# Optimization experiments

Hardware: AMD Instinct MI355X
Metric: run time of the kernel (lower is better)

## Reference

```python
import jax, jax.numpy as jnp
import numpy as np

N_NODES = 50000
N_EDGES = 800000
D = 128


def _gcn_conv(x, edge_index, W, b):
    """PyG GCNConv: out = D^{-1/2} (A + I) D^{-1/2} (x W) + b.

    edge_index[0] = source nodes, edge_index[1] = target nodes.
    Self-loops handled analytically instead of materializing them.
    """
    n = x.shape[0]
    src, dst = edge_index[0], edge_index[1]
    h = x @ W  # [N, out]
    # degree with self-loop: in-degree of target + 1
    deg = jax.ops.segment_sum(jnp.ones_like(dst, dtype=h.dtype), dst, num_segments=n) + 1.0
    dinv = jax.lax.rsqrt(deg)  # deg >= 1, safe
    norm = dinv[src] * dinv[dst]  # [E]
    msgs = norm[:, None] * h[src]  # [E, out]  (the big irregular-gather intermediate)
    agg = jax.ops.segment_sum(msgs, dst, num_segments=n)
    # self-loop contribution: norm = dinv[i]*dinv[i] = 1/deg
    agg = agg + h * (1.0 / deg)[:, None]
    return agg + b


def setup_inputs() -> dict:
    key = jax.random.key(0)
    k1, k2, k3, k4 = jax.random.split(key, 4)
    x = jax.random.normal(k1, (N_NODES, D), dtype=jnp.float32)
    edge_index = jax.random.randint(k2, (2, N_EDGES), 0, N_NODES, dtype=jnp.int64)
    scale = 1.0 / np.sqrt(D)
    W1 = jax.random.normal(k3, (D, D), dtype=jnp.float32) * scale
    W2 = jax.random.normal(k4, (D, D), dtype=jnp.float32) * scale
    b1 = jnp.zeros((D,), dtype=jnp.float32)
    b2 = jnp.zeros((D,), dtype=jnp.float32)
    return {"x": x, "edge_index": edge_index, "W1": W1, "b1": b1, "W2": W2, "b2": b2}


def reference(x, edge_index, W1, b1, W2, b2):
    h = _gcn_conv(x, edge_index, W1, b1)
    h = jax.nn.relu(h)  # dropout p=0.0 -> identity
    out = _gcn_conv(h, edge_index, W2, b2)
    return out
```

## Files before the change

### kernel.cpp

```cpp
#include <hip/hip_runtime.h>

#define DF 128
#define NBKT_MAX 256
#define CAP 8192

typedef unsigned int uint;
typedef unsigned short ushort;
typedef __attribute__((ext_vector_type(8))) short short8;
typedef __attribute__((ext_vector_type(4))) float f32x4;

union frag_u { uint4 u4; short8 s8; };

__device__ __forceinline__ uint f2u(float f) { return __float_as_uint(f); }
__device__ __forceinline__ ushort rne_bf16(float v) {
    uint u = __float_as_uint(v);
    u = u + 0x7FFFu + ((u >> 16) & 1u);
    return (ushort)(u >> 16);
}
__device__ __forceinline__ float bflo(uint u) { return __uint_as_float(u << 16); }
__device__ __forceinline__ float bfhi(uint u) { return __uint_as_float(u & 0xFFFF0000u); }

__global__ __launch_bounds__(256) void scatter_wprep(const int* __restrict__ src,
                                                     const int* __restrict__ dst,
                                                     int* __restrict__ ccur,
                                                     uint* __restrict__ ebuf,
                                                     int E, int NB, int SB,
                                                     const float* __restrict__ W1,
                                                     const float* __restrict__ W2,
                                                     uint4* __restrict__ Whi,
                                                     uint4* __restrict__ Wlo) {
    __shared__ int cnt[NBKT_MAX];
    __shared__ int base[NBKT_MAX];
    int t = threadIdx.x;
    if ((int)blockIdx.x < SB) {
        int e0 = blockIdx.x * 8192, e1 = min(E, e0 + 8192);
        for (int i = t; i < NB; i += 256) cnt[i] = 0;
        __syncthreads();
        for (int e = e0 + t; e < e1; e += 256) atomicAdd(&cnt[dst[e] >> 8], 1);
        __syncthreads();
        for (int i = t; i < NB; i += 256) base[i] = cnt[i] ? atomicAdd(&ccur[i], cnt[i]) : 0;
        __syncthreads();
        for (int e = e0 + t; e < e1; e += 256) {
            int d = dst[e];
            int b = d >> 8;
            int pos = atomicAdd(&base[b], 1);
            if (pos < CAP) ebuf[(size_t)b * CAP + pos] = ((uint)(d & 255) << 24) | (uint)src[e];
        }
    } else {
        int tt4 = ((int)blockIdx.x - SB) * 256 + t;
        int wsel = tt4 >> 11;
        int tt = tt4 & 2047;
        const float* W = wsel ? W2 : W1;
        int lane = tt & 63;
        int n  = ((tt >> 6) & 7) * 16 + (lane & 15);
        int k0 = (tt >> 9) * 32 + (lane >> 4) * 8;
        uint hi[4], lo[4];
#pragma unroll
        for (int p = 0; p < 4; ++p) {
            float f0 = W[(size_t)(k0 + 2 * p) * DF + n];
            float f1 = W[(size_t)(k0 + 2 * p + 1) * DF + n];
            uint u0 = f2u(f0), u1 = f2u(f1);
            hi[p] = (u1 & 0xFFFF0000u) | (u0 >> 16);
            float l0 = f0 - __uint_as_float(u0 & 0xFFFF0000u);
            float l1 = f1 - __uint_as_float(u1 & 0xFFFF0000u);
            lo[p] = (f2u(l1) & 0xFFFF0000u) | (f2u(l0) >> 16);
        }
        Whi[wsel * 2048 + tt] = make_uint4(hi[0], hi[1], hi[2], hi[3]);
        Wlo[wsel * 2048 + tt] = make_uint4(lo[0], lo[1], lo[2], lo[3]);
    }
}

__global__ __launch_bounds__(256) void sort_gemm1(const uint* __restrict__ ebuf,
                                                  const int* __restrict__ ccur,
                                                  int* __restrict__ rstart,
                                                  int* __restrict__ rend,
                                                  float* __restrict__ dinv,
                                                  ushort* __restrict__ srcs,
                                                  int* __restrict__ perm,
                                                  const float* __restrict__ A,
                                                  const uint4* __restrict__ Bhi,
                                                  const uint4* __restrict__ Blo,
                                                  ushort* __restrict__ Hq,
                                                  int NB, int N) {
    __shared__ int cnt[256];
    __shared__ int sp[256];
    __shared__ ushort prm[256];
    int t = threadIdx.x;
    if ((int)blockIdx.x < NB) {
        int b = blockIdx.x;
        int count = min(ccur[b], CAP);
        const uint* eb = ebuf + (size_t)b * CAP;
        cnt[t] = 0;
        __syncthreads();
        for (int j = t; j < count; j += 256) atomicAdd(&cnt[eb[j] >> 24], 1);
        __syncthreads();
        int v = cnt[t];
        sp[t] = v;
        __syncthreads();
        for (int off = 1; off < 256; off <<= 1) {
            int x = (t >= off) ? sp[t - off] : 0;
            __syncthreads();
            sp[t] += x;
            __syncthreads();
        }
        int ex = sp[t] - v;
        int node = b * 256 + t;
        if (node < N) {
            rstart[node] = b * CAP + ex;
            rend[node]   = b * CAP + ex + v;
            dinv[node] = rsqrtf((float)v + 1.0f);
        }
        int rank = 0;
#pragma unroll 8
        for (int u = 0; u < 256; ++u) {
            int du = cnt[u];
            rank += (du > v) || (du == v && u < t);
        }
        prm[rank] = (ushort)t;
        sp[t] = ex;
        __syncthreads();
        perm[b * 256 + t] = b * 256 + (int)prm[t];
        for (int j = t; j < count; j += 256) {
            uint e = eb[j];
            int pos = atomicAdd(&sp[e >> 24], 1);
            srcs[(size_t)b * CAP + pos] = (ushort)(e & 0xFFFFFFu);
        }
    } else {
        const int lane = t & 63;
        const int w = t >> 6;
        const int l15 = lane & 15, quad = lane >> 4;
        const int rowbase = ((int)blockIdx.x - NB) * 128 + w * 32;
        const int M = N;

        f32x4 acc[2][8];
#pragma unroll
        for (int rt = 0; rt < 2; ++rt)
#pragma unroll
            for (int ct = 0; ct < 8; ++ct) acc[rt][ct] = (f32x4){0.f, 0.f, 0.f, 0.f};

        for (int q = 0; q < 4; ++q) {
            frag_u ah[2], al[2];
#pragma unroll
            for (int rt = 0; rt < 2; ++rt) {
                int m = rowbase + rt * 16 + l15;
                if (m >= M) m = M - 1;
                const float* ap = A + (size_t)m * DF + q * 32 + quad * 8;
                float4 v0 = *(const float4*)ap;
                float4 v1 = *(const float4*)(ap + 4);
                float f[8] = {v0.x, v0.y, v0.z, v0.w, v1.x, v1.y, v1.z, v1.w};
                uint hi[4], lo[4];
#pragma unroll
                for (int p = 0; p < 4; ++p) {
                    uint u0 = f2u(f[2 * p]), u1 = f2u(f[2 * p + 1]);
                    hi[p] = (u1 & 0xFFFF0000u) | (u0 >> 16);
                    float l0 = f[2 * p]     - __uint_as_float(u0 & 0xFFFF0000u);
                    float l1 = f[2 * p + 1] - __uint_as_float(u1 & 0xFFFF0000u);
                    lo[p] = (f2u(l1) & 0xFFFF0000u) | (f2u(l0) >> 16);
                }
                ah[rt].u4 = make_uint4(hi[0], hi[1], hi[2], hi[3]);
                al[rt].u4 = make_uint4(lo[0], lo[1], lo[2], lo[3]);
            }
#pragma unroll
            for (int ct = 0; ct < 8; ++ct) {
                frag_u bh, bl;
                bh.u4 = Bhi[(q * 8 + ct) * 64 + lane];
                bl.u4 = Blo[(q * 8 + ct) * 64 + lane];
#pragma unroll
                for (int rt = 0; rt < 2; ++rt) {
                    acc[rt][ct] = __builtin_amdgcn_mfma_f32_16x16x32_bf16(al[rt].s8, bh.s8, acc[rt][ct], 0, 0, 0);
                    acc[rt][ct] = __builtin_amdgcn_mfma_f32_16x16x32_bf16(ah[rt].s8, bl.s8, acc[rt][ct], 0, 0, 0);
                    acc[rt][ct] = __builtin_amdgcn_mfma_f32_16x16x32_bf16(ah[rt].s8, bh.s8, acc[rt][ct], 0, 0, 0);
                }
            }
        }
#pragma unroll
        for (int rt = 0; rt < 2; ++rt)
#pragma unroll
            for (int reg = 0; reg < 4; ++reg) {
                int row = rowbase + rt * 16 + quad * 4 + reg;
                if (row < M) {
#pragma unroll
                    for (int ct = 0; ct < 8; ++ct)
                        Hq[((size_t)(ct >> 1) * M + row) * 32 + (ct & 1) * 16 + l15] =
                            rne_bf16(acc[rt][ct][reg]);
                }
            }
    }
}

__global__ __launch_bounds__(256) void gemm_bf16A(const ushort* __restrict__ A,
                                                  const uint4* __restrict__ Bhi,
                                                  const uint4* __restrict__ Blo,
                                                  const float* __restrict__ dinv,
                                                  ushort* __restrict__ Hq, int M) {
    const int lane = threadIdx.x & 63;
    const int w = threadIdx.x >> 6;
    const int l15 = lane & 15, quad = lane >> 4;
    const int rowbase = blockIdx.x * 128 + w * 32;

    f32x4 acc[2][8];
#pragma unroll
    for (int rt = 0; rt < 2; ++rt)
#pragma unroll
        for (int ct = 0; ct < 8; ++ct) acc[rt][ct] = (f32x4){0.f, 0.f, 0.f, 0.f};

    for (int q = 0; q < 4; ++q) {
        frag_u a[2];
#pragma unroll
        for (int rt = 0; rt < 2; ++rt) {
            int m = rowbase + rt * 16 + l15;
            if (m >= M) m = M - 1;
            const ushort* ap = A + ((size_t)q * M + m) * 32 + quad * 8;
            a[rt].u4 = *(const uint4*)ap;
        }
#pragma unroll
        for (int ct = 0; ct < 8; ++ct) {
            frag_u bh, bl;
            bh.u4 = Bhi[(q * 8 + ct) * 64 + lane];
            bl.u4 = Blo[(q * 8 + ct) * 64 + lane];
#pragma unroll
            for (int rt = 0; rt < 2; ++rt) {
                acc[rt][ct] = __builtin_amdgcn_mfma_f32_16x16x32_bf16(a[rt].s8, bl.s8, acc[rt][ct], 0, 0, 0);
                acc[rt][ct] = __builtin_amdgcn_mfma_f32_16x16x32_bf16(a[rt].s8, bh.s8, acc[rt][ct], 0, 0, 0);
            }
        }
    }
#pragma unroll
    for (int rt = 0; rt < 2; ++rt)
#pragma unroll
        for (int reg = 0; reg < 4; ++reg) {
            int row = rowbase + rt * 16 + quad * 4 + reg;
            if (row < M) {
                float di = dinv[row];
#pragma unroll
                for (int ct = 0; ct < 8; ++ct)
                    Hq[((size_t)(ct >> 1) * M + row) * 32 + (ct & 1) * 16 + l15] =
                        rne_bf16(acc[rt][ct][reg] * di);
            }
        }
}

template<bool L1>
__global__ __launch_bounds__(256) void quarter_gather(const uint4* __restrict__ H4,
                                                      const float* __restrict__ dinv,
                                                      const int* __restrict__ rstart,
                                                      const int* __restrict__ rend,
                                                      const ushort* __restrict__ srcs,
                                                      const int* __restrict__ perm,
                                                      const float* __restrict__ bias,
                                                      void* __restrict__ outv, int N) {
    int t = threadIdx.x;
    int bid = blockIdx.x;
    int sub = bid & 7;
    int q = sub >> 1;
    int slot = (bid >> 3) * 128 + (sub & 1) * 64 + (t >> 2);
    int n = perm[slot];
    if (n >= N) return;
    int l = t & 3;
    const uint4* Hq4 = H4 + (size_t)q * N * 4;

    float4 bb0 = ((const float4*)bias)[q * 8 + l * 2];
    float4 bb1 = ((const float4*)bias)[q * 8 + l * 2 + 1];

    float di = dinv[n];
    uint4 self = Hq4[(size_t)n * 4 + l];
    float sc = L1 ? di : 1.0f;
    float a0 = bflo(self.x) * sc, a1 = bfhi(self.x) * sc, a2 = bflo(self.y) * sc, a3 = bfhi(self.y) * sc;
    float a4 = bflo(self.z) * sc, a5 = bfhi(self.z) * sc, a6 = bflo(self.w) * sc, a7 = bfhi(self.w) * sc;

    int j = rstart[n], end = rend[n];
    for (; j + 4 <= end; j += 4) {
        int s0 = srcs[j], s1 = srcs[j + 1], s2 = srcs[j + 2], s3 = srcs[j + 3];
        uint4 v0 = Hq4[(size_t)s0 * 4 + l];
        uint4 v1 = Hq4[(size_t)s1 * 4 + l];
        uint4 v2 = Hq4[(size_t)s2 * 4 + l];
        uint4 v3 = Hq4[(size_t)s3 * 4 + l];
        if constexpr (L1) {
            float d0 = dinv[s0], d1 = dinv[s1], d2 = dinv[s2], d3 = dinv[s3];
            a0 = fmaf(bflo(v0.x), d0, a0); a0 = fmaf(bflo(v1.x), d1, a0);
            a0 = fmaf(bflo(v2.x), d2, a0); a0 = fmaf(bflo(v3.x), d3, a0);
            a1 = fmaf(bfhi(v0.x), d0, a1); a1 = fmaf(bfhi(v1.x), d1, a1);
            a1 = fmaf(bfhi(v2.x), d2, a1); a1 = fmaf(bfhi(v3.x), d3, a1);
            a2 = fmaf(bflo(v0.y), d0, a2); a2 = fmaf(bflo(v1.y), d1, a2);
            a2 = fmaf(bflo(v2.y), d2, a2); a2 = fmaf(bflo(v3.y), d3, a2);
            a3 = fmaf(bfhi(v0.y), d0, a3); a3 = fmaf(bfhi(v1.y), d1, a3);
            a3 = fmaf(bfhi(v2.y), d2, a3); a3 = fmaf(bfhi(v3.y), d3, a3);
            a4 = fmaf(bflo(v0.z), d0, a4); a4 = fmaf(bflo(v1.z), d1, a4);
            a4 = fmaf(bflo(v2.z), d2, a4); a4 = fmaf(bflo(v3.z), d3, a4);
            a5 = fmaf(bfhi(v0.z), d0, a5); a5 = fmaf(bfhi(v1.z), d1, a5);
            a5 = fmaf(bfhi(v2.z), d2, a5); a5 = fmaf(bfhi(v3.z), d3, a5);
            a6 = fmaf(bflo(v0.w), d0, a6); a6 = fmaf(bflo(v1.w), d1, a6);
            a6 = fmaf(bflo(v2.w), d2, a6); a6 = fmaf(bflo(v3.w), d3, a6);
            a7 = fmaf(bfhi(v0.w), d0, a7); a7 = fmaf(bfhi(v1.w), d1, a7);
            a7 = fmaf(bfhi(v2.w), d2, a7); a7 = fmaf(bfhi(v3.w), d3, a7);
        } else {
            a0 += (bflo(v0.x) + bflo(v1.x)) + (bflo(v2.x) + bflo(v3.x));
            a1 += (bfhi(v0.x) + bfhi(v1.x)) + (bfhi(v2.x) + bfhi(v3.x));
            a2 += (bflo(v0.y) + bflo(v1.y)) + (bflo(v2.y) + bflo(v3.y));
            a3 += (bfhi(v0.y) + bfhi(v1.y)) + (bfhi(v2.y) + bfhi(v3.y));
            a4 += (bflo(v0.z) + bflo(v1.z)) + (bflo(v2.z) + bflo(v3.z));
            a5 += (bfhi(v0.z) + bfhi(v1.z)) + (bfhi(v2.z) + bfhi(v3.z));
            a6 += (bflo(v0.w) + bflo(v1.w)) + (bflo(v2.w) + bflo(v3.w));
            a7 += (bfhi(v0.w) + bfhi(v1.w)) + (bfhi(v2.w) + bfhi(v3.w));
        }
    }
    for (; j < end; ++j) {
        int s = srcs[j];
        uint4 v = Hq4[(size_t)s * 4 + l];
        if constexpr (L1) {
            float d = dinv[s];
            a0 = fmaf(bflo(v.x), d, a0); a1 = fmaf(bfhi(v.x), d, a1);
            a2 = fmaf(bflo(v.y), d, a2); a3 = fmaf(bfhi(v.y), d, a3);
            a4 = fmaf(bflo(v.z), d, a4); a5 = fmaf(bfhi(v.z), d, a5);
            a6 = fmaf(bflo(v.w), d, a6); a7 = fmaf(bfhi(v.w), d, a7);
        } else {
            a0 += bflo(v.x); a1 += bfhi(v.x); a2 += bflo(v.y); a3 += bfhi(v.y);
            a4 += bflo(v.z); a5 += bfhi(v.z); a6 += bflo(v.w); a7 += bfhi(v.w);
        }
    }
    float o0 = fmaf(a0, di, bb0.x), o1 = fmaf(a1, di, bb0.y);
    float o2 = fmaf(a2, di, bb0.z), o3 = fmaf(a3, di, bb0.w);
    float o4 = fmaf(a4, di, bb1.x), o5 = fmaf(a5, di, bb1.y);
    float o6 = fmaf(a6, di, bb1.z), o7 = fmaf(a7, di, bb1.w);
    if (L1) {
        o0 = fmaxf(o0, 0.f); o1 = fmaxf(o1, 0.f); o2 = fmaxf(o2, 0.f); o3 = fmaxf(o3, 0.f);
        o4 = fmaxf(o4, 0.f); o5 = fmaxf(o5, 0.f); o6 = fmaxf(o6, 0.f); o7 = fmaxf(o7, 0.f);
        uint4 pk;
        pk.x = (uint)rne_bf16(o0) | ((uint)rne_bf16(o1) << 16);
        pk.y = (uint)rne_bf16(o2) | ((uint)rne_bf16(o3) << 16);
        pk.z = (uint)rne_bf16(o4) | ((uint)rne_bf16(o5) << 16);
        pk.w = (uint)rne_bf16(o6) | ((uint)rne_bf16(o7) << 16);
        ((uint4*)outv)[((size_t)q * N + n) * 4 + l] = pk;
    } else {
        float4* op = (float4*)((float*)outv + (size_t)n * DF + q * 32 + l * 8);
        op[0] = make_float4(o0, o1, o2, o3);
        op[1] = make_float4(o4, o5, o6, o7);
    }
}

extern "C" void kernel_launch(void* const* d_in, const int* in_sizes, int n_in,
                              void* d_out, int out_size, void* d_ws, size_t ws_size,
                              hipStream_t stream) {
    const float* x  = (const float*)d_in[0];
    const int*   ei = (const int*)d_in[1];
    const float* W1 = (const float*)d_in[2];
    const float* b1 = (const float*)d_in[3];
    const float* W2 = (const float*)d_in[4];
    const float* b2 = (const float*)d_in[5];

    const int N = in_sizes[0] / DF;
    const int E = in_sizes[1] / 2;
    const int* src = ei;
    const int* dstp = ei + E;
    const int NB = (N + 255) >> 8;
    const int SB = (E + 8191) / 8192;

    float* out = (float*)d_out;
    char* ws = (char*)d_ws;
    size_t off = 0;
    auto carve = [&](size_t bytes) { void* p = ws + off; off += (bytes + 255) & ~(size_t)255; return p; };
    ushort* Hq     = (ushort*)carve((size_t)N * DF * sizeof(ushort));
    ushort* Z1     = (ushort*)carve((size_t)N * DF * sizeof(ushort));
    float*  dinv   = (float*)carve((size_t)N * sizeof(float));
    int*    rstart = (int*)carve((size_t)N * sizeof(int));
    int*    rend   = (int*)carve((size_t)N * sizeof(int));
    int*    perm   = (int*)carve((size_t)NB * 256 * sizeof(int));
    uint*   ebuf   = (uint*)carve((size_t)NB * CAP * sizeof(uint));
    ushort* srcs   = (ushort*)carve((size_t)NB * CAP * sizeof(ushort));
    int*    ccur   = (int*)carve(NBKT_MAX * sizeof(int));
    uint4*  Whi    = (uint4*)carve(2 * 2048 * sizeof(uint4));
    uint4*  Wlo    = (uint4*)carve(2 * 2048 * sizeof(uint4));

    const int gemm_b = (N + 127) / 128;
    const int gath_b = ((N + 127) / 128) * 8;

    hipMemsetAsync(ccur, 0, NBKT_MAX * sizeof(int), stream);
    scatter_wprep<<<SB + 16, 256, 0, stream>>>(src, dstp, ccur, ebuf, E, NB, SB, W1, W2, Whi, Wlo);

    sort_gemm1<<<NB + gemm_b, 256, 0, stream>>>(ebuf, ccur, rstart, rend, dinv, srcs, perm,
                                                x, Whi, Wlo, Hq, NB, N);

    quarter_gather<true><<<gath_b, 256, 0, stream>>>((const uint4*)Hq, dinv, rstart, rend,
                                                     srcs, perm, b1, Z1, N);

    gemm_bf16A<<<gemm_b, 256, 0, stream>>>(Z1, Whi + 2048, Wlo + 2048, dinv, Hq, N);
    quarter_gather<false><<<gath_b, 256, 0, stream>>>((const uint4*)Hq, dinv, rstart, rend,
                                                      srcs, perm, b2, out, N);
}
```

Baseline: 234.9 us.

## Pad CSR rows to 8, vectorize edge loads, drop degree-sorted permutation

The scatter kernel now processes smaller edge chunks with each thread loading 8 edges through int4 vector loads. In the sort stage each node's edge segment is padded to a multiple of 8, which aligns row starts so the gather can read 8 source indices with one uint4 load and issue 8 row fetches at once. The degree-sorted permutation used for load balancing is removed, so gather blocks map nodes directly. This trades warp-level balance across nodes of differing degree for more memory-level parallelism and fewer index loads. Padding also uses more bucket capacity, and any edges beyond CAP are now dropped silently.

```diff
diff --git a/kernel.cpp b/kernel.cpp
--- a/kernel.cpp
+++ b/kernel.cpp
@@ -3,6 +3,7 @@
 #define DF 128
 #define NBKT_MAX 256
 #define CAP 8192
+#define SCHUNK 2048
 
 typedef unsigned int uint;
 typedef unsigned short ushort;
@@ -33,19 +34,34 @@
     __shared__ int base[NBKT_MAX];
     int t = threadIdx.x;
     if ((int)blockIdx.x < SB) {
-        int e0 = blockIdx.x * 8192, e1 = min(E, e0 + 8192);
+        int e0 = blockIdx.x * SCHUNK;
+        int eb0 = e0 + t * 8;
+        int lim = min(E - eb0, 8);
+        int d[8], s[8];
+        if (lim == 8) {
+            int4 d0 = *(const int4*)(dst + eb0), d1 = *(const int4*)(dst + eb0 + 4);
+            int4 s0 = *(const int4*)(src + eb0), s1 = *(const int4*)(src + eb0 + 4);
+            d[0] = d0.x; d[1] = d0.y; d[2] = d0.z; d[3] = d0.w;
+            d[4] = d1.x; d[5] = d1.y; d[6] = d1.z; d[7] = d1.w;
+            s[0] = s0.x; s[1] = s0.y; s[2] = s0.z; s[3] = s0.w;
+            s[4] = s1.x; s[5] = s1.y; s[6] = s1.z; s[7] = s1.w;
+        } else {
+            for (int i = 0; i < 8; ++i) { d[i] = 0; s[i] = 0; }
+            for (int i = 0; i < lim; ++i) { d[i] = dst[eb0 + i]; s[i] = src[eb0 + i]; }
+        }
         for (int i = t; i < NB; i += 256) cnt[i] = 0;
         __syncthreads();
-        for (int e = e0 + t; e < e1; e += 256) atomicAdd(&cnt[dst[e] >> 8], 1);
+        for (int i = 0; i < 8; ++i)
+            if (i < lim) atomicAdd(&cnt[d[i] >> 8], 1);
         __syncthreads();
         for (int i = t; i < NB; i += 256) base[i] = cnt[i] ? atomicAdd(&ccur[i], cnt[i]) : 0;
         __syncthreads();
-        for (int e = e0 + t; e < e1; e += 256) {
-            int d = dst[e];
-            int b = d >> 8;
-            int pos = atomicAdd(&base[b], 1);
-            if (pos < CAP) ebuf[(size_t)b * CAP + pos] = ((uint)(d & 255) << 24) | (uint)src[e];
-        }
+        for (int i = 0; i < 8; ++i)
+            if (i < lim) {
+                int b = d[i] >> 8;
+                int pos = atomicAdd(&base[b], 1);
+                if (pos < CAP) ebuf[(size_t)b * CAP + pos] = ((uint)(d[i] & 255) << 24) | (uint)s[i];
+            }
     } else {
         int tt4 = ((int)blockIdx.x - SB) * 256 + t;
         int wsel = tt4 >> 11;
@@ -76,7 +92,6 @@
                                                   int* __restrict__ rend,
                                                   float* __restrict__ dinv,
                                                   ushort* __restrict__ srcs,
-                                                  int* __restrict__ perm,
                                                   const float* __restrict__ A,
                                                   const uint4* __restrict__ Bhi,
                                                   const uint4* __restrict__ Blo,
@@ -84,7 +99,6 @@
                                                   int NB, int N) {
     __shared__ int cnt[256];
     __shared__ int sp[256];
-    __shared__ ushort prm[256];
     int t = threadIdx.x;
     if ((int)blockIdx.x < NB) {
         int b = blockIdx.x;
@@ -95,7 +109,8 @@
         for (int j = t; j < count; j += 256) atomicAdd(&cnt[eb[j] >> 24], 1);
         __syncthreads();
         int v = cnt[t];
-        sp[t] = v;
+        int pv = (v + 7) & ~7;
+        sp[t] = pv;
         __syncthreads();
         for (int off = 1; off < 256; off <<= 1) {
             int x = (t >= off) ? sp[t - off] : 0;
@@ -103,27 +118,19 @@
             sp[t] += x;
             __syncthreads();
         }
-        int ex = sp[t] - v;
+        int ex = sp[t] - pv;
         int node = b * 256 + t;
         if (node < N) {
             rstart[node] = b * CAP + ex;
             rend[node]   = b * CAP + ex + v;
             dinv[node] = rsqrtf((float)v + 1.0f);
         }
-        int rank = 0;
-#pragma unroll 8
-        for (int u = 0; u < 256; ++u) {
-            int du = cnt[u];
-            rank += (du > v) || (du == v && u < t);
-        }
-        prm[rank] = (ushort)t;
         sp[t] = ex;
         __syncthreads();
-        perm[b * 256 + t] = b * 256 + (int)prm[t];
         for (int j = t; j < count; j += 256) {
             uint e = eb[j];
             int pos = atomicAdd(&sp[e >> 24], 1);
-            srcs[(size_t)b * CAP + pos] = (ushort)(e & 0xFFFFFFu);
+            if (pos < CAP) srcs[(size_t)b * CAP + pos] = (ushort)(e & 0xFFFFFFu);
         }
     } else {
         const int lane = t & 63;
@@ -246,15 +253,13 @@
                                                       const int* __restrict__ rstart,
                                                       const int* __restrict__ rend,
                                                       const ushort* __restrict__ srcs,
-                                                      const int* __restrict__ perm,
                                                       const float* __restrict__ bias,
                                                       void* __restrict__ outv, int N) {
     int t = threadIdx.x;
     int bid = blockIdx.x;
     int sub = bid & 7;
     int q = sub >> 1;
-    int slot = (bid >> 3) * 128 + (sub & 1) * 64 + (t >> 2);
-    int n = perm[slot];
+    int n = (bid >> 3) * 128 + (sub & 1) * 64 + (t >> 2);
     if (n >= N) return;
     int l = t & 3;
     const uint4* Hq4 = H4 + (size_t)q * N * 4;
@@ -269,39 +274,35 @@
     float a4 = bflo(self.z) * sc, a5 = bfhi(self.z) * sc, a6 = bflo(self.w) * sc, a7 = bfhi(self.w) * sc;
 
     int j = rstart[n], end = rend[n];
-    for (; j + 4 <= end; j += 4) {
-        int s0 = srcs[j], s1 = srcs[j + 1], s2 = srcs[j + 2], s3 = srcs[j + 3];
-        uint4 v0 = Hq4[(size_t)s0 * 4 + l];
-        uint4 v1 = Hq4[(size_t)s1 * 4 + l];
-        uint4 v2 = Hq4[(size_t)s2 * 4 + l];
-        uint4 v3 = Hq4[(size_t)s3 * 4 + l];
+    for (; j + 8 <= end; j += 8) {
+        uint4 sv = *(const uint4*)(srcs + j);
+        int si[8];
+        si[0] = sv.x & 0xFFFF; si[1] = sv.x >> 16;
+        si[2] = sv.y & 0xFFFF; si[3] = sv.y >> 16;
+        si[4] = sv.z & 0xFFFF; si[5] = sv.z >> 16;
+        si[6] = sv.w & 0xFFFF; si[7] = sv.w >> 16;
+        uint4 v[8];
+#pragma unroll
+        for (int i = 0; i < 8; ++i) v[i] = Hq4[(size_t)si[i] * 4 + l];
         if constexpr (L1) {
-            float d0 = dinv[s0], d1 = dinv[s1], d2 = dinv[s2], d3 = dinv[s3];
-            a0 = fmaf(bflo(v0.x), d0, a0); a0 = fmaf(bflo(v1.x), d1, a0);
-            a0 = fmaf(bflo(v2.x), d2, a0); a0 = fmaf(bflo(v3.x), d3, a0);
-            a1 = fmaf(bfhi(v0.x), d0, a1); a1 = fmaf(bfhi(v1.x), d1, a1);
-            a1 = fmaf(bfhi(v2.x), d2, a1); a1 = fmaf(bfhi(v3.x), d3, a1);
-            a2 = fmaf(bflo(v0.y), d0, a2); a2 = fmaf(bflo(v1.y), d1, a2);
-            a2 = fmaf(bflo(v2.y), d2, a2); a2 = fmaf(bflo(v3.y), d3, a2);
-            a3 = fmaf(bfhi(v0.y), d0, a3); a3 = fmaf(bfhi(v1.y), d1, a3);
-            a3 = fmaf(bfhi(v2.y), d2, a3); a3 = fmaf(bfhi(v3.y), d3, a3);
-            a4 = fmaf(bflo(v0.z), d0, a4); a4 = fmaf(bflo(v1.z), d1, a4);
-            a4 = fmaf(bflo(v2.z), d2, a4); a4 = fmaf(bflo(v3.z), d3, a4);
-            a5 = fmaf(bfhi(v0.z), d0, a5); a5 = fmaf(bfhi(v1.z), d1, a5);
-            a5 = fmaf(bfhi(v2.z), d2, a5); a5 = fmaf(bfhi(v3.z), d3, a5);
-            a6 = fmaf(bflo(v0.w), d0, a6); a6 = fmaf(bflo(v1.w), d1, a6);
-            a6 = fmaf(bflo(v2.w), d2, a6); a6 = fmaf(bflo(v3.w), d3, a6);
-            a7 = fmaf(bfhi(v0.w), d0, a7); a7 = fmaf(bfhi(v1.w), d1, a7);
-            a7 = fmaf(bfhi(v2.w), d2, a7); a7 = fmaf(bfhi(v3.w), d3, a7);
+            float dd[8];
+#pragma unroll
+            for (int i = 0; i < 8; ++i) dd[i] = dinv[si[i]];
+#pragma unroll
+            for (int i = 0; i < 8; ++i) {
+                a0 = fmaf(bflo(v[i].x), dd[i], a0); a1 = fmaf(bfhi(v[i].x), dd[i], a1);
+                a2 = fmaf(bflo(v[i].y), dd[i], a2); a3 = fmaf(bfhi(v[i].y), dd[i], a3);
+                a4 = fmaf(bflo(v[i].z), dd[i], a4); a5 = fmaf(bfhi(v[i].z), dd[i], a5);
+                a6 = fmaf(bflo(v[i].w), dd[i], a6); a7 = fmaf(bfhi(v[i].w), dd[i], a7);
+            }
         } else {
-            a0 += (bflo(v0.x) + bflo(v1.x)) + (bflo(v2.x) + bflo(v3.x));
-            a1 += (bfhi(v0.x) + bfhi(v1.x)) + (bfhi(v2.x) + bfhi(v3.x));
-            a2 += (bflo(v0.y) + bflo(v1.y)) + (bflo(v2.y) + bflo(v3.y));
-            a3 += (bfhi(v0.y) + bfhi(v1.y)) + (bfhi(v2.y) + bfhi(v3.y));
-            a4 += (bflo(v0.z) + bflo(v1.z)) + (bflo(v2.z) + bflo(v3.z));
-            a5 += (bfhi(v0.z) + bfhi(v1.z)) + (bfhi(v2.z) + bfhi(v3.z));
-            a6 += (bflo(v0.w) + bflo(v1.w)) + (bflo(v2.w) + bflo(v3.w));
-            a7 += (bfhi(v0.w) + bfhi(v1.w)) + (bfhi(v2.w) + bfhi(v3.w));
+#pragma unroll
+            for (int i = 0; i < 8; ++i) {
+                a0 += bflo(v[i].x); a1 += bfhi(v[i].x);
+                a2 += bflo(v[i].y); a3 += bfhi(v[i].y);
+                a4 += bflo(v[i].z); a5 += bfhi(v[i].z);
+                a6 += bflo(v[i].w); a7 += bfhi(v[i].w);
+            }
         }
     }
     for (; j < end; ++j) {
@@ -353,7 +354,7 @@
     const int* src = ei;
     const int* dstp = ei + E;
     const int NB = (N + 255) >> 8;
-    const int SB = (E + 8191) / 8192;
+    const int SB = (E + SCHUNK - 1) / SCHUNK;
 
     float* out = (float*)d_out;
     char* ws = (char*)d_ws;
@@ -364,7 +365,6 @@
     float*  dinv   = (float*)carve((size_t)N * sizeof(float));
     int*    rstart = (int*)carve((size_t)N * sizeof(int));
     int*    rend   = (int*)carve((size_t)N * sizeof(int));
-    int*    perm   = (int*)carve((size_t)NB * 256 * sizeof(int));
     uint*   ebuf   = (uint*)carve((size_t)NB * CAP * sizeof(uint));
     ushort* srcs   = (ushort*)carve((size_t)NB * CAP * sizeof(ushort));
     int*    ccur   = (int*)carve(NBKT_MAX * sizeof(int));
@@ -377,13 +377,13 @@
     hipMemsetAsync(ccur, 0, NBKT_MAX * sizeof(int), stream);
     scatter_wprep<<<SB + 16, 256, 0, stream>>>(src, dstp, ccur, ebuf, E, NB, SB, W1, W2, Whi, Wlo);
 
-    sort_gemm1<<<NB + gemm_b, 256, 0, stream>>>(ebuf, ccur, rstart, rend, dinv, srcs, perm,
+    sort_gemm1<<<NB + gemm_b, 256, 0, stream>>>(ebuf, ccur, rstart, rend, dinv, srcs,
                                                 x, Whi, Wlo, Hq, NB, N);
 
     quarter_gather<true><<<gath_b, 256, 0, stream>>>((const uint4*)Hq, dinv, rstart, rend,
-                                                     srcs, perm, b1, Z1, N);
+                                                     srcs, b1, Z1, N);
 
     gemm_bf16A<<<gemm_b, 256, 0, stream>>>(Z1, Whi + 2048, Wlo + 2048, dinv, Hq, N);
     quarter_gather<false><<<gath_b, 256, 0, stream>>>((const uint4*)Hq, dinv, rstart, rend,
-                                                      srcs, perm, b2, out, N);
-}
+                                                      srcs, b2, out, N);
+}
```

After: 201.3 us. -14.3%, faster.
